# Kernel optimization log

Measured on AMD Instinct MI355X. Metric: run time of the kernel, lower is better.

The kernel has to match this reference:

```python
import jax, jax.numpy as jnp
import numpy as np

COMPRESSION = 2  # max-pool factor along flattened spatial axis for phi and g


def setup_inputs() -> dict:
    key = jax.random.key(0)
    ks = jax.random.split(key, 5)
    B, C, H, W = 4, 64, 96, 96
    Ci = 32  # intermediate_dim = C // 2
    s = 1.0 / np.sqrt(C)
    return {
        "x": jax.random.normal(ks[0], (B, C, H, W), dtype=jnp.float32),
        "w_theta": jax.random.normal(ks[1], (Ci, C), dtype=jnp.float32) * s,
        "b_theta": jnp.zeros((Ci,), dtype=jnp.float32),
        "w_phi": jax.random.normal(ks[2], (Ci, C), dtype=jnp.float32) * s,
        "b_phi": jnp.zeros((Ci,), dtype=jnp.float32),
        "w_g": jax.random.normal(ks[3], (Ci, C), dtype=jnp.float32) * s,
        "b_g": jnp.zeros((Ci,), dtype=jnp.float32),
        "w_out": jax.random.normal(ks[4], (C, Ci), dtype=jnp.float32) * (1.0 / np.sqrt(Ci)),
        "b_out": jnp.zeros((C,), dtype=jnp.float32),
    }


def reference(x, w_theta, b_theta, w_phi, b_phi, w_g, b_g, w_out, b_out):
    B, C, H, W = x.shape
    N = H * W
    xf = x.reshape(B, C, N).transpose(0, 2, 1)            # [B, N, C]
    # 1x1 conv projections == channel matmuls
    theta = xf @ w_theta.T + b_theta                      # [B, N, Ci]
    phi = xf @ w_phi.T + b_phi                            # [B, N, Ci]
    g = xf @ w_g.T + b_g                                  # [B, N, Ci]
    # compression: max-pool (kernel=stride=COMPRESSION) along flattened spatial axis
    Ci = theta.shape[-1]
    phi = phi.reshape(B, N // COMPRESSION, COMPRESSION, Ci).max(axis=2)  # [B, N/c, Ci]
    g = g.reshape(B, N // COMPRESSION, COMPRESSION, Ci).max(axis=2)      # [B, N/c, Ci]
    # embedded-gaussian affinity + softmax
    attn = jax.nn.softmax(jnp.einsum('bnc,bmc->bnm', theta, phi), axis=-1)  # [B, N, N/c]
    y = jnp.einsum('bnm,bmc->bnc', attn, g)               # [B, N, Ci]
    out = y @ w_out.T + b_out                             # [B, N, C]
    out = out.transpose(0, 2, 1).reshape(B, C, H, W)
    return out + x  # residual
```

## Files before the change

kernel.cpp:

```cpp
#include <hip/hip_runtime.h>
#include <hip/hip_bf16.h>


#define NQ 9216
#define MM 4608
#define LOG2E 1.44269504088896340736f

typedef __attribute__((ext_vector_type(8))) short bf16x8;
typedef __attribute__((ext_vector_type(4))) float f32x4;
typedef __attribute__((ext_vector_type(4))) unsigned short u16x4;

static __device__ __forceinline__ unsigned pk2(float a, float b) {
    __hip_bfloat162 h = __float22bfloat162_rn(make_float2(a, b));
    return *reinterpret_cast<unsigned*>(&h);
}

__global__ __launch_bounds__(256, 4) void proj_kernel(
    const float* __restrict__ x,
    const float* __restrict__ wt, const float* __restrict__ bt,
    const float* __restrict__ wp, const float* __restrict__ bp,
    const float* __restrict__ wg, const float* __restrict__ bg,
    unsigned short* __restrict__ theta, unsigned short* __restrict__ phi,
    unsigned short* __restrict__ gT, float* __restrict__ pzero)
{
    __shared__ unsigned short gst[32 * 20];

    const int tid  = threadIdx.x;
    const int wid  = tid >> 6;
    const int lane = tid & 63;
    const int q = lane >> 4;
    const int c = lane & 15;
    const int role = wid >> 1;
    const int sub  = wid & 1;

    {
        const int gs = gridDim.x * blockDim.x;
        float4 z4 = {0.f, 0.f, 0.f, 0.f};
        for (int i = blockIdx.x * blockDim.x + tid; i < 304128; i += gs)
            ((float4*)pzero)[i] = z4;
    }

    const int b     = blockIdx.x / 288;
    const int rem   = blockIdx.x % 288;
    const int n0blk = rem * 32;
    const int n0    = n0blk + sub * 16;

    bf16x8 af[2];
#pragma unroll
    for (int ks = 0; ks < 2; ++ks) {
        unsigned* ap = (unsigned*)&af[ks];
#pragma unroll
        for (int j2 = 0; j2 < 4; ++j2) {
            float x0 = x[(b * 64 + ks * 32 + q * 8 + j2 * 2) * NQ + n0 + c];
            float x1 = x[(b * 64 + ks * 32 + q * 8 + j2 * 2 + 1) * NQ + n0 + c];
            ap[j2] = pk2(x0, x1);
        }
    }

    if (role == 0) {
        bf16x8 wf[2][2];
        float bias[2];
#pragma unroll
        for (int ct = 0; ct < 2; ++ct) {
            bias[ct] = bt[ct * 16 + c];
#pragma unroll
            for (int ks = 0; ks < 2; ++ks) {
                const float* wsrc = wt + (ct * 16 + c) * 64 + ks * 32 + q * 8;
                f32x4 w0 = *(const f32x4*)wsrc;
                f32x4 w1 = *(const f32x4*)(wsrc + 4);
                unsigned* wk = (unsigned*)&wf[ct][ks];
                wk[0] = pk2(w0[0], w0[1]); wk[1] = pk2(w0[2], w0[3]);
                wk[2] = pk2(w1[0], w1[1]); wk[3] = pk2(w1[2], w1[3]);
            }
        }
#pragma unroll
        for (int ct = 0; ct < 2; ++ct) {
            f32x4 acc = {0.f, 0.f, 0.f, 0.f};
            acc = __builtin_amdgcn_mfma_f32_16x16x32_bf16(af[0], wf[ct][0], acc, 0, 0, 0);
            acc = __builtin_amdgcn_mfma_f32_16x16x32_bf16(af[1], wf[ct][1], acc, 0, 0, 0);
            const int ci = ct * 16 + c;
            unsigned pv0 = pk2((acc[0] + bias[ct]) * LOG2E, (acc[1] + bias[ct]) * LOG2E);
            unsigned pv1 = pk2((acc[2] + bias[ct]) * LOG2E, (acc[3] + bias[ct]) * LOG2E);
            theta[(b * NQ + n0 + 4 * q + 0) * 32 + ci] = (unsigned short)pv0;
            theta[(b * NQ + n0 + 4 * q + 1) * 32 + ci] = (unsigned short)(pv0 >> 16);
            theta[(b * NQ + n0 + 4 * q + 2) * 32 + ci] = (unsigned short)pv1;
            theta[(b * NQ + n0 + 4 * q + 3) * 32 + ci] = (unsigned short)(pv1 >> 16);
        }
    } else {
        const float* Wm[2] = {wp, wg};
        const float* Bm[2] = {bp, bg};
        bf16x8 wf[2][2][2];
        float bias[2][2];
#pragma unroll
        for (int p = 0; p < 2; ++p) {
#pragma unroll
            for (int ct = 0; ct < 2; ++ct) {
                bias[p][ct] = Bm[p][ct * 16 + c];
#pragma unroll
                for (int ks = 0; ks < 2; ++ks) {
                    const float* wsrc = Wm[p] + (ct * 16 + c) * 64 + ks * 32 + q * 8;
                    f32x4 w0 = *(const f32x4*)wsrc;
                    f32x4 w1 = *(const f32x4*)(wsrc + 4);
                    unsigned* wk = (unsigned*)&wf[p][ct][ks];
                    wk[0] = pk2(w0[0], w0[1]); wk[1] = pk2(w0[2], w0[3]);
                    wk[2] = pk2(w1[0], w1[1]); wk[3] = pk2(w1[2], w1[3]);
                }
            }
        }
#pragma unroll
        for (int p = 0; p < 2; ++p) {
#pragma unroll
            for (int ct = 0; ct < 2; ++ct) {
                f32x4 acc = {0.f, 0.f, 0.f, 0.f};
                acc = __builtin_amdgcn_mfma_f32_16x16x32_bf16(af[0], wf[p][ct][0], acc, 0, 0, 0);
                acc = __builtin_amdgcn_mfma_f32_16x16x32_bf16(af[1], wf[p][ct][1], acc, 0, 0, 0);
#pragma unroll
                for (int r = 0; r < 4; ++r) acc[r] += bias[p][ct];
                const int ci = ct * 16 + c;
                unsigned pv = pk2(fmaxf(acc[0], acc[1]), fmaxf(acc[2], acc[3]));
                if (p == 0) {
                    const int m0 = (n0 >> 1) + 2 * q;
                    phi[(b * MM + m0) * 32 + ci]     = (unsigned short)pv;
                    phi[(b * MM + m0 + 1) * 32 + ci] = (unsigned short)(pv >> 16);
                } else {
                    *(unsigned int*)(gst + ci * 20 + sub * 8 + 2 * q) = pv;
                }
            }
        }
    }

    __syncthreads();
    if (tid < 128) {
        const int ci = tid >> 2;
        const int m4 = (tid & 3) * 4;
        u16x4 v = *(const u16x4*)(gst + ci * 20 + m4);
        *(u16x4*)(gT + (b * 32 + ci) * MM + (n0blk >> 1) + m4) = v;
    }
}

__global__ __launch_bounds__(128, 4) void attn_kernel(
    const unsigned short* __restrict__ theta, const unsigned short* __restrict__ phi,
    const unsigned short* __restrict__ gT,
    float* __restrict__ pacc, float* __restrict__ plsum)
{
    __shared__ unsigned short pld[2][64 * 64];

    const int tid  = threadIdx.x;
    const int w    = tid >> 6;
    const int lane = tid & 63;
    const int q  = lane >> 4;
    const int c  = lane & 15;
    const int xr = (c & 7) << 3;

    const int ks  = blockIdx.x / 288;
    const int rem = blockIdx.x % 288;
    const int b   = rem / 72;
    const int nb  = (rem % 72) * 128 + w * 64;

    bf16x8 qf[4];
#pragma unroll
    for (int rt = 0; rt < 4; ++rt)
        qf[rt] = *(const bf16x8*)(theta + (b * NQ + nb + rt * 16 + c) * 32 + q * 8);

    bf16x8 onef;
    {
        unsigned v = (c == 0) ? 0x3F803F80u : 0u;
        unsigned* op = (unsigned*)&onef;
        op[0] = v; op[1] = v; op[2] = v; op[3] = v;
    }

    const unsigned short* phiB = phi + (size_t)b * MM * 32;
    const unsigned short* gTB  = gT + (size_t)b * 32 * MM;
    unsigned short* myp = pld[w];

    f32x4 acc[4][2];
    f32x4 lacc[4];
#pragma unroll
    for (int rt = 0; rt < 4; ++rt) {
        lacc[rt] = (f32x4){0.f, 0.f, 0.f, 0.f};
#pragma unroll
        for (int s2 = 0; s2 < 2; ++s2) acc[rt][s2] = (f32x4){0.f, 0.f, 0.f, 0.f};
    }

    const int mt0 = ks * 6;
    bf16x8 kf[4], vf[2][2];

#pragma unroll
    for (int mct = 0; mct < 4; ++mct)
        kf[mct] = *(const bf16x8*)(phiB + (mt0 * 64 + mct * 16 + c) * 32 + q * 8);
#pragma unroll
    for (int s2 = 0; s2 < 2; ++s2)
#pragma unroll
        for (int st = 0; st < 2; ++st)
            vf[s2][st] = *(const bf16x8*)(gTB + (s2 * 16 + c) * MM + mt0 * 64 + st * 32 + q * 8);
#pragma unroll
    for (int mct = 0; mct < 4; ++mct) {
#pragma unroll
        for (int rt = 0; rt < 4; ++rt) {
            f32x4 z = {0.f, 0.f, 0.f, 0.f};
            f32x4 s = __builtin_amdgcn_mfma_f32_16x16x32_bf16(kf[mct], qf[rt], z, 0, 0, 0);
            uint2 hv = {pk2(__builtin_amdgcn_exp2f(s[0]), __builtin_amdgcn_exp2f(s[1])),
                        pk2(__builtin_amdgcn_exp2f(s[2]), __builtin_amdgcn_exp2f(s[3]))};
            *(uint2*)(myp + ((rt * 16 + c) << 6) + ((mct * 16 + 4 * q) ^ xr)) = hv;
        }
    }

    for (int mi = 1; mi < 6; ++mi) {
        const int m0 = (mt0 + mi) * 64;

#pragma unroll
        for (int mct = 0; mct < 4; ++mct)
            kf[mct] = *(const bf16x8*)(phiB + (m0 + mct * 16 + c) * 32 + q * 8);

#pragma unroll
        for (int rt = 0; rt < 4; ++rt) {
#pragma unroll
            for (int st = 0; st < 2; ++st) {
                bf16x8 pf = *(const bf16x8*)(myp + ((rt * 16 + c) << 6) + ((st * 32 + q * 8) ^ xr));
#pragma unroll
                for (int s2 = 0; s2 < 2; ++s2)
                    acc[rt][s2] = __builtin_amdgcn_mfma_f32_16x16x32_bf16(vf[s2][st], pf, acc[rt][s2], 0, 0, 0);
                lacc[rt] = __builtin_amdgcn_mfma_f32_16x16x32_bf16(onef, pf, lacc[rt], 0, 0, 0);
            }
        }

#pragma unroll
        for (int s2 = 0; s2 < 2; ++s2)
#pragma unroll
            for (int st = 0; st < 2; ++st)
                vf[s2][st] = *(const bf16x8*)(gTB + (s2 * 16 + c) * MM + m0 + st * 32 + q * 8);

#pragma unroll
        for (int mct = 0; mct < 4; ++mct) {
#pragma unroll
            for (int rt = 0; rt < 4; ++rt) {
                f32x4 z = {0.f, 0.f, 0.f, 0.f};
                f32x4 s = __builtin_amdgcn_mfma_f32_16x16x32_bf16(kf[mct], qf[rt], z, 0, 0, 0);
                uint2 hv = {pk2(__builtin_amdgcn_exp2f(s[0]), __builtin_amdgcn_exp2f(s[1])),
                            pk2(__builtin_amdgcn_exp2f(s[2]), __builtin_amdgcn_exp2f(s[3]))};
                *(uint2*)(myp + ((rt * 16 + c) << 6) + ((mct * 16 + 4 * q) ^ xr)) = hv;
            }
        }
    }

#pragma unroll
    for (int rt = 0; rt < 4; ++rt) {
#pragma unroll
        for (int st = 0; st < 2; ++st) {
            bf16x8 pf = *(const bf16x8*)(myp + ((rt * 16 + c) << 6) + ((st * 32 + q * 8) ^ xr));
#pragma unroll
            for (int s2 = 0; s2 < 2; ++s2)
                acc[rt][s2] = __builtin_amdgcn_mfma_f32_16x16x32_bf16(vf[s2][st], pf, acc[rt][s2], 0, 0, 0);
            lacc[rt] = __builtin_amdgcn_mfma_f32_16x16x32_bf16(onef, pf, lacc[rt], 0, 0, 0);
        }
    }

#pragma unroll
    for (int rt = 0; rt < 4; ++rt)
#pragma unroll
        for (int s2 = 0; s2 < 2; ++s2)
#pragma unroll
            for (int r = 0; r < 4; ++r)
                atomicAdd(&pacc[(size_t)(b * 32 + s2 * 16 + 4 * q + r) * NQ + nb + rt * 16 + c],
                          acc[rt][s2][r]);
    if (lane < 16) {
#pragma unroll
        for (int rt = 0; rt < 4; ++rt)
            atomicAdd(&plsum[(size_t)b * NQ + nb + rt * 16 + lane], lacc[rt][0]);
    }
}

__global__ __launch_bounds__(128, 4) void reduce_kernel(
    const float* __restrict__ pacc, const float* __restrict__ plsum,
    const float* __restrict__ w_out, const float* __restrict__ b_out,
    const float* __restrict__ x, float* __restrict__ out)
{
    __shared__ unsigned short yld[32 * 36];

    const int tid = threadIdx.x;
    const int b   = blockIdx.x / 288;
    const int nb  = (blockIdx.x % 288) * 32;

    {
        const int ci = tid >> 2;
        const int n8 = (tid & 3) * 8;
        const float* pr = pacc + (size_t)(b * 32 + ci) * NQ + nb + n8;
        f32x4 a0 = *(const f32x4*)pr;
        f32x4 a1 = *(const f32x4*)(pr + 4);
        const float* lr = plsum + (size_t)b * NQ + nb + n8;
        f32x4 l0 = *(const f32x4*)lr;
        f32x4 l1 = *(const f32x4*)(lr + 4);
        uint2 v0 = {pk2(a0[0] / l0[0], a0[1] / l0[1]), pk2(a0[2] / l0[2], a0[3] / l0[3])};
        uint2 v1 = {pk2(a1[0] / l1[0], a1[1] / l1[1]), pk2(a1[2] / l1[2], a1[3] / l1[3])};
        *(uint2*)(yld + ci * 36 + n8)     = v0;
        *(uint2*)(yld + ci * 36 + n8 + 4) = v1;
    }
    __syncthreads();

    const int w    = tid >> 6;
    const int lane = tid & 63;
    const int q = lane >> 4;
    const int c = lane & 15;

    bf16x8 wof[4];
#pragma unroll
    for (int ct = 0; ct < 4; ++ct) {
        const float* wsrc = w_out + (ct * 16 + c) * 32 + q * 8;
        f32x4 w0 = *(const f32x4*)wsrc;
        f32x4 w1 = *(const f32x4*)(wsrc + 4);
        unsigned* wk = (unsigned*)&wof[ct];
        wk[0] = pk2(w0[0], w0[1]); wk[1] = pk2(w0[2], w0[3]);
        wk[2] = pk2(w1[0], w1[1]); wk[3] = pk2(w1[2], w1[3]);
    }

    bf16x8 yf;
    {
        unsigned short* yp = (unsigned short*)&yf;
#pragma unroll
        for (int j = 0; j < 8; ++j)
            yp[j] = yld[(q * 8 + j) * 36 + w * 16 + c];
    }

#pragma unroll
    for (int ct = 0; ct < 4; ++ct) {
        f32x4 z = {0.f, 0.f, 0.f, 0.f};
        f32x4 o = __builtin_amdgcn_mfma_f32_16x16x32_bf16(wof[ct], yf, z, 0, 0, 0);
#pragma unroll
        for (int r = 0; r < 4; ++r) {
            const int chn = ct * 16 + 4 * q + r;
            const size_t addr = (size_t)(b * 64 + chn) * NQ + nb + w * 16 + c;
            out[addr] = o[r] + b_out[chn] + x[addr];
        }
    }
}

extern "C" void kernel_launch(void* const* d_in, const int* in_sizes, int n_in,
                              void* d_out, int out_size, void* d_ws, size_t ws_size,
                              hipStream_t stream) {
    const float* x       = (const float*)d_in[0];
    const float* w_theta = (const float*)d_in[1];
    const float* b_theta = (const float*)d_in[2];
    const float* w_phi   = (const float*)d_in[3];
    const float* b_phi   = (const float*)d_in[4];
    const float* w_g     = (const float*)d_in[5];
    const float* b_g     = (const float*)d_in[6];
    const float* w_out   = (const float*)d_in[7];
    const float* b_out   = (const float*)d_in[8];
    float* out = (float*)d_out;

    unsigned short* theta = (unsigned short*)d_ws;
    unsigned short* phi   = theta + 4 * NQ * 32;
    unsigned short* gT    = phi + 4 * MM * 32;
    float* pacc  = (float*)(gT + 4 * 32 * MM);
    float* plsum = pacc + (size_t)4 * 32 * NQ;

    proj_kernel<<<1152, 256, 0, stream>>>(x, w_theta, b_theta, w_phi, b_phi,
                                          w_g, b_g, theta, phi, gT, pacc);
    attn_kernel<<<12 * 288, 128, 0, stream>>>(theta, phi, gT, pacc, plsum);
    reduce_kernel<<<1152, 128, 0, stream>>>(pacc, plsum, w_out, b_out, x, out);
}
```

Measured before the change: 151.4 us.

## Fuse output projection into attention kernel via last-block counter and resplit keys

```diff
diff --git a/kernel.cpp b/kernel.cpp
--- a/kernel.cpp
+++ b/kernel.cpp
@@ -36,7 +36,7 @@
     {
         const int gs = gridDim.x * blockDim.x;
         float4 z4 = {0.f, 0.f, 0.f, 0.f};
-        for (int i = blockIdx.x * blockDim.x + tid; i < 304128; i += gs)
+        for (int i = blockIdx.x * blockDim.x + tid; i < 304200; i += gs)
             ((float4*)pzero)[i] = z4;
     }
 
@@ -138,12 +138,15 @@
     }
 }
 
-__global__ __launch_bounds__(128, 4) void attn_kernel(
+__global__ __launch_bounds__(128, 3) void attn_kernel(
     const unsigned short* __restrict__ theta, const unsigned short* __restrict__ phi,
-    const unsigned short* __restrict__ gT,
-    float* __restrict__ pacc, float* __restrict__ plsum)
+    const unsigned short* __restrict__ gT, const float* __restrict__ w_out,
+    const float* __restrict__ b_out, const float* __restrict__ x,
+    float* __restrict__ pacc, float* __restrict__ plsum, int* __restrict__ cnt,
+    float* __restrict__ out)
 {
     __shared__ unsigned short pld[2][64 * 64];
+    __shared__ int lastSh;
 
     const int tid  = threadIdx.x;
     const int w    = tid >> 6;
@@ -155,7 +158,8 @@
     const int ks  = blockIdx.x / 288;
     const int rem = blockIdx.x % 288;
     const int b   = rem / 72;
-    const int nb  = (rem % 72) * 128 + w * 64;
+    const int qb  = rem % 72;
+    const int nb  = qb * 128 + w * 64;
 
     bf16x8 qf[4];
 #pragma unroll
@@ -182,7 +186,7 @@
         for (int s2 = 0; s2 < 2; ++s2) acc[rt][s2] = (f32x4){0.f, 0.f, 0.f, 0.f};
     }
 
-    const int mt0 = ks * 6;
+    const int mt0 = ks * 9;
     bf16x8 kf[4], vf[2][2];
 
 #pragma unroll
@@ -205,7 +209,7 @@
         }
     }
 
-    for (int mi = 1; mi < 6; ++mi) {
+    for (int mi = 1; mi < 9; ++mi) {
         const int m0 = (mt0 + mi) * 64;
 
 #pragma unroll
@@ -268,39 +272,16 @@
         for (int rt = 0; rt < 4; ++rt)
             atomicAdd(&plsum[(size_t)b * NQ + nb + rt * 16 + lane], lacc[rt][0]);
     }
-}
-
-__global__ __launch_bounds__(128, 4) void reduce_kernel(
-    const float* __restrict__ pacc, const float* __restrict__ plsum,
-    const float* __restrict__ w_out, const float* __restrict__ b_out,
-    const float* __restrict__ x, float* __restrict__ out)
-{
-    __shared__ unsigned short yld[32 * 36];
-
-    const int tid = threadIdx.x;
-    const int b   = blockIdx.x / 288;
-    const int nb  = (blockIdx.x % 288) * 32;
-
-    {
-        const int ci = tid >> 2;
-        const int n8 = (tid & 3) * 8;
-        const float* pr = pacc + (size_t)(b * 32 + ci) * NQ + nb + n8;
-        f32x4 a0 = *(const f32x4*)pr;
-        f32x4 a1 = *(const f32x4*)(pr + 4);
-        const float* lr = plsum + (size_t)b * NQ + nb + n8;
-        f32x4 l0 = *(const f32x4*)lr;
-        f32x4 l1 = *(const f32x4*)(lr + 4);
-        uint2 v0 = {pk2(a0[0] / l0[0], a0[1] / l0[1]), pk2(a0[2] / l0[2], a0[3] / l0[3])};
-        uint2 v1 = {pk2(a1[0] / l1[0], a1[1] / l1[1]), pk2(a1[2] / l1[2], a1[3] / l1[3])};
-        *(uint2*)(yld + ci * 36 + n8)     = v0;
-        *(uint2*)(yld + ci * 36 + n8 + 4) = v1;
-    }
+
     __syncthreads();
-
-    const int w    = tid >> 6;
-    const int lane = tid & 63;
-    const int q = lane >> 4;
-    const int c = lane & 15;
+    if (tid == 0) {
+        __threadfence();
+        int old = __hip_atomic_fetch_add(&cnt[rem], 1, __ATOMIC_ACQ_REL,
+                                         __HIP_MEMORY_SCOPE_AGENT);
+        lastSh = (old == 7);
+    }
+    __syncthreads();
+    if (!lastSh) return;
 
     bf16x8 wof[4];
 #pragma unroll
@@ -313,24 +294,46 @@
         wk[2] = pk2(w1[0], w1[1]); wk[3] = pk2(w1[2], w1[3]);
     }
 
-    bf16x8 yf;
-    {
-        unsigned short* yp = (unsigned short*)&yf;
-#pragma unroll
-        for (int j = 0; j < 8; ++j)
-            yp[j] = yld[(q * 8 + j) * 36 + w * 16 + c];
-    }
-
-#pragma unroll
-    for (int ct = 0; ct < 4; ++ct) {
-        f32x4 z = {0.f, 0.f, 0.f, 0.f};
-        f32x4 o = __builtin_amdgcn_mfma_f32_16x16x32_bf16(wof[ct], yf, z, 0, 0, 0);
-#pragma unroll
-        for (int r = 0; r < 4; ++r) {
-            const int chn = ct * 16 + 4 * q + r;
-            const size_t addr = (size_t)(b * 64 + chn) * NQ + nb + w * 16 + c;
-            out[addr] = o[r] + b_out[chn] + x[addr];
-        }
+    unsigned short* yld = pld[0];
+    for (int chunk = 0; chunk < 4; ++chunk) {
+        const int nb0 = qb * 128 + chunk * 32;
+        {
+            const int ci = tid >> 2;
+            const int n8 = (tid & 3) * 8;
+            const float* pr = pacc + (size_t)(b * 32 + ci) * NQ + nb0 + n8;
+            const float* lr = plsum + (size_t)b * NQ + nb0 + n8;
+            float a[8], l[8];
+#pragma unroll
+            for (int j = 0; j < 8; ++j) {
+                a[j] = __hip_atomic_load(pr + j, __ATOMIC_RELAXED, __HIP_MEMORY_SCOPE_AGENT);
+                l[j] = __hip_atomic_load(lr + j, __ATOMIC_RELAXED, __HIP_MEMORY_SCOPE_AGENT);
+            }
+            uint2 v0 = {pk2(a[0] / l[0], a[1] / l[1]), pk2(a[2] / l[2], a[3] / l[3])};
+            uint2 v1 = {pk2(a[4] / l[4], a[5] / l[5]), pk2(a[6] / l[6], a[7] / l[7])};
+            *(uint2*)(yld + ci * 36 + n8)     = v0;
+            *(uint2*)(yld + ci * 36 + n8 + 4) = v1;
+        }
+        __syncthreads();
+
+        bf16x8 yf;
+        {
+            unsigned short* yp = (unsigned short*)&yf;
+#pragma unroll
+            for (int j = 0; j < 8; ++j)
+                yp[j] = yld[(q * 8 + j) * 36 + w * 16 + c];
+        }
+#pragma unroll
+        for (int ct = 0; ct < 4; ++ct) {
+            f32x4 z = {0.f, 0.f, 0.f, 0.f};
+            f32x4 o = __builtin_amdgcn_mfma_f32_16x16x32_bf16(wof[ct], yf, z, 0, 0, 0);
+#pragma unroll
+            for (int r = 0; r < 4; ++r) {
+                const int chn = ct * 16 + 4 * q + r;
+                const size_t addr = (size_t)(b * 64 + chn) * NQ + nb0 + w * 16 + c;
+                out[addr] = o[r] + b_out[chn] + x[addr];
+            }
+        }
+        __syncthreads();
     }
 }
 
@@ -353,9 +356,10 @@
     unsigned short* gT    = phi + 4 * MM * 32;
     float* pacc  = (float*)(gT + 4 * 32 * MM);
     float* plsum = pacc + (size_t)4 * 32 * NQ;
+    int*   cnt   = (int*)(plsum + (size_t)4 * NQ);
 
     proj_kernel<<<1152, 256, 0, stream>>>(x, w_theta, b_theta, w_phi, b_phi,
                                           w_g, b_g, theta, phi, gT, pacc);
-    attn_kernel<<<12 * 288, 128, 0, stream>>>(theta, phi, gT, pacc, plsum);
-    reduce_kernel<<<1152, 128, 0, stream>>>(pacc, plsum, w_out, b_out, x, out);
+    attn_kernel<<<8 * 288, 128, 0, stream>>>(theta, phi, gT, w_out, b_out, x,
+                                             pacc, plsum, cnt, out);
 }
```

After: 232.0 us. 53.2% more time.

## Split attention tile into two row-halves to interleave softmax-exp and PV MFMAs

Applied to the files above, without the earlier changes.

```diff
diff --git a/kernel.cpp b/kernel.cpp
--- a/kernel.cpp
+++ b/kernel.cpp
@@ -13,6 +13,42 @@
 static __device__ __forceinline__ unsigned pk2(float a, float b) {
     __hip_bfloat162 h = __float22bfloat162_rn(make_float2(a, b));
     return *reinterpret_cast<unsigned*>(&h);
+}
+
+template <int R0>
+static __device__ __forceinline__ void s_half(
+    const bf16x8* kf, const bf16x8* qf, unsigned short* stg,
+    int c, int q, int xr)
+{
+#pragma unroll
+    for (int mct = 0; mct < 4; ++mct) {
+#pragma unroll
+        for (int rr = 0; rr < 2; ++rr) {
+            f32x4 z = {0.f, 0.f, 0.f, 0.f};
+            f32x4 s = __builtin_amdgcn_mfma_f32_16x16x32_bf16(kf[mct], qf[R0 + rr], z, 0, 0, 0);
+            uint2 hv = {pk2(__builtin_amdgcn_exp2f(s[0]), __builtin_amdgcn_exp2f(s[1])),
+                        pk2(__builtin_amdgcn_exp2f(s[2]), __builtin_amdgcn_exp2f(s[3]))};
+            *(uint2*)(stg + ((rr * 16 + c) << 6) + ((mct * 16 + 4 * q) ^ xr)) = hv;
+        }
+    }
+}
+
+template <int R0>
+static __device__ __forceinline__ void pv_half(
+    const bf16x8 (&vf)[2][2], const bf16x8& onef, const unsigned short* stg,
+    int c, int q, int xr, f32x4 (&acc)[4][2], f32x4 (&lacc)[4])
+{
+#pragma unroll
+    for (int rr = 0; rr < 2; ++rr) {
+#pragma unroll
+        for (int st = 0; st < 2; ++st) {
+            bf16x8 pf = *(const bf16x8*)(stg + ((rr * 16 + c) << 6) + ((st * 32 + q * 8) ^ xr));
+#pragma unroll
+            for (int s2 = 0; s2 < 2; ++s2)
+                acc[R0 + rr][s2] = __builtin_amdgcn_mfma_f32_16x16x32_bf16(vf[s2][st], pf, acc[R0 + rr][s2], 0, 0, 0);
+            lacc[R0 + rr] = __builtin_amdgcn_mfma_f32_16x16x32_bf16(onef, pf, lacc[R0 + rr], 0, 0, 0);
+        }
+    }
 }
 
 __global__ __launch_bounds__(256, 4) void proj_kernel(
@@ -138,12 +174,12 @@
     }
 }
 
-__global__ __launch_bounds__(128, 4) void attn_kernel(
+__global__ __launch_bounds__(128, 3) void attn_kernel(
     const unsigned short* __restrict__ theta, const unsigned short* __restrict__ phi,
     const unsigned short* __restrict__ gT,
     float* __restrict__ pacc, float* __restrict__ plsum)
 {
-    __shared__ unsigned short pld[2][64 * 64];
+    __shared__ unsigned short pld[2][2][32 * 64];
 
     const int tid  = threadIdx.x;
     const int w    = tid >> 6;
@@ -171,7 +207,8 @@
 
     const unsigned short* phiB = phi + (size_t)b * MM * 32;
     const unsigned short* gTB  = gT + (size_t)b * 32 * MM;
-    unsigned short* myp = pld[w];
+    unsigned short* stg0 = pld[w][0];
+    unsigned short* stg1 = pld[w][1];
 
     f32x4 acc[4][2];
     f32x4 lacc[4];
@@ -182,78 +219,43 @@
         for (int s2 = 0; s2 < 2; ++s2) acc[rt][s2] = (f32x4){0.f, 0.f, 0.f, 0.f};
     }
 
-    const int mt0 = ks * 6;
+    const int mt0 = ks * 9;
     bf16x8 kf[4], vf[2][2];
 
 #pragma unroll
     for (int mct = 0; mct < 4; ++mct)
         kf[mct] = *(const bf16x8*)(phiB + (mt0 * 64 + mct * 16 + c) * 32 + q * 8);
+    s_half<0>(kf, qf, stg0, c, q, xr);
 #pragma unroll
     for (int s2 = 0; s2 < 2; ++s2)
 #pragma unroll
         for (int st = 0; st < 2; ++st)
             vf[s2][st] = *(const bf16x8*)(gTB + (s2 * 16 + c) * MM + mt0 * 64 + st * 32 + q * 8);
-#pragma unroll
-    for (int mct = 0; mct < 4; ++mct) {
-#pragma unroll
-        for (int rt = 0; rt < 4; ++rt) {
-            f32x4 z = {0.f, 0.f, 0.f, 0.f};
-            f32x4 s = __builtin_amdgcn_mfma_f32_16x16x32_bf16(kf[mct], qf[rt], z, 0, 0, 0);
-            uint2 hv = {pk2(__builtin_amdgcn_exp2f(s[0]), __builtin_amdgcn_exp2f(s[1])),
-                        pk2(__builtin_amdgcn_exp2f(s[2]), __builtin_amdgcn_exp2f(s[3]))};
-            *(uint2*)(myp + ((rt * 16 + c) << 6) + ((mct * 16 + 4 * q) ^ xr)) = hv;
-        }
-    }
-
-    for (int mi = 1; mi < 6; ++mi) {
-        const int m0 = (mt0 + mi) * 64;
-
-#pragma unroll
-        for (int mct = 0; mct < 4; ++mct)
-            kf[mct] = *(const bf16x8*)(phiB + (m0 + mct * 16 + c) * 32 + q * 8);
-
-#pragma unroll
-        for (int rt = 0; rt < 4; ++rt) {
-#pragma unroll
-            for (int st = 0; st < 2; ++st) {
-                bf16x8 pf = *(const bf16x8*)(myp + ((rt * 16 + c) << 6) + ((st * 32 + q * 8) ^ xr));
-#pragma unroll
-                for (int s2 = 0; s2 < 2; ++s2)
-                    acc[rt][s2] = __builtin_amdgcn_mfma_f32_16x16x32_bf16(vf[s2][st], pf, acc[rt][s2], 0, 0, 0);
-                lacc[rt] = __builtin_amdgcn_mfma_f32_16x16x32_bf16(onef, pf, lacc[rt], 0, 0, 0);
-            }
-        }
-
+    s_half<2>(kf, qf, stg1, c, q, xr);
+#pragma unroll
+    for (int mct = 0; mct < 4; ++mct)
+        kf[mct] = *(const bf16x8*)(phiB + ((mt0 + 1) * 64 + mct * 16 + c) * 32 + q * 8);
+    pv_half<0>(vf, onef, stg0, c, q, xr, acc, lacc);
+
+    for (int mi = 1; mi < 9; ++mi) {
+        const int m0  = (mt0 + mi) * 64;
+        const int m0n = (mt0 + (mi < 8 ? mi + 1 : mi)) * 64;
+
+        s_half<0>(kf, qf, stg0, c, q, xr);
+        pv_half<2>(vf, onef, stg1, c, q, xr, acc, lacc);
 #pragma unroll
         for (int s2 = 0; s2 < 2; ++s2)
 #pragma unroll
             for (int st = 0; st < 2; ++st)
                 vf[s2][st] = *(const bf16x8*)(gTB + (s2 * 16 + c) * MM + m0 + st * 32 + q * 8);
-
-#pragma unroll
-        for (int mct = 0; mct < 4; ++mct) {
-#pragma unroll
-            for (int rt = 0; rt < 4; ++rt) {
-                f32x4 z = {0.f, 0.f, 0.f, 0.f};
-                f32x4 s = __builtin_amdgcn_mfma_f32_16x16x32_bf16(kf[mct], qf[rt], z, 0, 0, 0);
-                uint2 hv = {pk2(__builtin_amdgcn_exp2f(s[0]), __builtin_amdgcn_exp2f(s[1])),
-                            pk2(__builtin_amdgcn_exp2f(s[2]), __builtin_amdgcn_exp2f(s[3]))};
-                *(uint2*)(myp + ((rt * 16 + c) << 6) + ((mct * 16 + 4 * q) ^ xr)) = hv;
-            }
-        }
-    }
-
-#pragma unroll
-    for (int rt = 0; rt < 4; ++rt) {
-#pragma unroll
-        for (int st = 0; st < 2; ++st) {
-            bf16x8 pf = *(const bf16x8*)(myp + ((rt * 16 + c) << 6) + ((st * 32 + q * 8) ^ xr));
-#pragma unroll
-            for (int s2 = 0; s2 < 2; ++s2)
-                acc[rt][s2] = __builtin_amdgcn_mfma_f32_16x16x32_bf16(vf[s2][st], pf, acc[rt][s2], 0, 0, 0);
-            lacc[rt] = __builtin_amdgcn_mfma_f32_16x16x32_bf16(onef, pf, lacc[rt], 0, 0, 0);
-        }
-    }
+        s_half<2>(kf, qf, stg1, c, q, xr);
+#pragma unroll
+        for (int mct = 0; mct < 4; ++mct)
+            kf[mct] = *(const bf16x8*)(phiB + (m0n + mct * 16 + c) * 32 + q * 8);
+        pv_half<0>(vf, onef, stg0, c, q, xr, acc, lacc);
+    }
+
+    pv_half<2>(vf, onef, stg1, c, q, xr, acc, lacc);
 
 #pragma unroll
     for (int rt = 0; rt < 4; ++rt)
@@ -356,6 +358,6 @@
 
     proj_kernel<<<1152, 256, 0, stream>>>(x, w_theta, b_theta, w_phi, b_phi,
                                           w_g, b_g, theta, phi, gT, pacc);
-    attn_kernel<<<12 * 288, 128, 0, stream>>>(theta, phi, gT, pacc, plsum);
+    attn_kernel<<<8 * 288, 128, 0, stream>>>(theta, phi, gT, pacc, plsum);
     reduce_kernel<<<1152, 128, 0, stream>>>(pacc, plsum, w_out, b_out, x, out);
 }
```

Result: no change. 149.3 us (-1.4%).

## Halve query tile per wave, lengthen key split, rotate key-tile start order

Applied to the files above, without the earlier changes.

```diff
diff --git a/kernel.cpp b/kernel.cpp
--- a/kernel.cpp
+++ b/kernel.cpp
@@ -138,12 +138,12 @@
     }
 }
 
-__global__ __launch_bounds__(128, 4) void attn_kernel(
+__global__ __launch_bounds__(128, 6) void attn_kernel(
     const unsigned short* __restrict__ theta, const unsigned short* __restrict__ phi,
     const unsigned short* __restrict__ gT,
     float* __restrict__ pacc, float* __restrict__ plsum)
 {
-    __shared__ unsigned short pld[2][64 * 64];
+    __shared__ unsigned short pld[2][32 * 64];
 
     const int tid  = threadIdx.x;
     const int w    = tid >> 6;
@@ -152,14 +152,15 @@
     const int c  = lane & 15;
     const int xr = (c & 7) << 3;
 
-    const int ks  = blockIdx.x / 288;
-    const int rem = blockIdx.x % 288;
-    const int b   = rem / 72;
-    const int nb  = (rem % 72) * 128 + w * 64;
-
-    bf16x8 qf[4];
-#pragma unroll
-    for (int rt = 0; rt < 4; ++rt)
+    const int ks  = blockIdx.x / 576;
+    const int rem = blockIdx.x % 576;
+    const int b   = rem / 144;
+    const int qb  = rem % 144;
+    const int nb  = qb * 64 + w * 32;
+
+    bf16x8 qf[2];
+#pragma unroll
+    for (int rt = 0; rt < 2; ++rt)
         qf[rt] = *(const bf16x8*)(theta + (b * NQ + nb + rt * 16 + c) * 32 + q * 8);
 
     bf16x8 onef;
@@ -173,81 +174,102 @@
     const unsigned short* gTB  = gT + (size_t)b * 32 * MM;
     unsigned short* myp = pld[w];
 
-    f32x4 acc[4][2];
-    f32x4 lacc[4];
-#pragma unroll
-    for (int rt = 0; rt < 4; ++rt) {
+    unsigned short* wadr[4];
+#pragma unroll
+    for (int mct = 0; mct < 4; ++mct)
+        wadr[mct] = myp + (c << 6) + ((mct * 16 + 4 * q) ^ xr);
+    const unsigned short* radr[2];
+#pragma unroll
+    for (int st = 0; st < 2; ++st)
+        radr[st] = myp + (c << 6) + ((st * 32 + q * 8) ^ xr);
+
+    const int ofsK = c * 32 + q * 8;
+    const int ofsV = c * MM + q * 8;
+
+    f32x4 acc[2][2];
+    f32x4 lacc[2];
+#pragma unroll
+    for (int rt = 0; rt < 2; ++rt) {
         lacc[rt] = (f32x4){0.f, 0.f, 0.f, 0.f};
 #pragma unroll
         for (int s2 = 0; s2 < 2; ++s2) acc[rt][s2] = (f32x4){0.f, 0.f, 0.f, 0.f};
     }
 
-    const int mt0 = ks * 6;
+    const int mt0 = ks * 9;
+    const int rot = blockIdx.x % 9;
     bf16x8 kf[4], vf[2][2];
 
-#pragma unroll
-    for (int mct = 0; mct < 4; ++mct)
-        kf[mct] = *(const bf16x8*)(phiB + (mt0 * 64 + mct * 16 + c) * 32 + q * 8);
-#pragma unroll
-    for (int s2 = 0; s2 < 2; ++s2)
-#pragma unroll
-        for (int st = 0; st < 2; ++st)
-            vf[s2][st] = *(const bf16x8*)(gTB + (s2 * 16 + c) * MM + mt0 * 64 + st * 32 + q * 8);
-#pragma unroll
-    for (int mct = 0; mct < 4; ++mct) {
-#pragma unroll
-        for (int rt = 0; rt < 4; ++rt) {
-            f32x4 z = {0.f, 0.f, 0.f, 0.f};
-            f32x4 s = __builtin_amdgcn_mfma_f32_16x16x32_bf16(kf[mct], qf[rt], z, 0, 0, 0);
-            uint2 hv = {pk2(__builtin_amdgcn_exp2f(s[0]), __builtin_amdgcn_exp2f(s[1])),
-                        pk2(__builtin_amdgcn_exp2f(s[2]), __builtin_amdgcn_exp2f(s[3]))};
-            *(uint2*)(myp + ((rt * 16 + c) << 6) + ((mct * 16 + 4 * q) ^ xr)) = hv;
-        }
-    }
-
-    for (int mi = 1; mi < 6; ++mi) {
-        const int m0 = (mt0 + mi) * 64;
-
+    {
+        const int mt = mt0 + rot;
+        const unsigned short* pk = phiB + mt * 2048;
+        const unsigned short* pv = gTB + mt * 64;
 #pragma unroll
         for (int mct = 0; mct < 4; ++mct)
-            kf[mct] = *(const bf16x8*)(phiB + (m0 + mct * 16 + c) * 32 + q * 8);
-
-#pragma unroll
-        for (int rt = 0; rt < 4; ++rt) {
-#pragma unroll
-            for (int st = 0; st < 2; ++st) {
-                bf16x8 pf = *(const bf16x8*)(myp + ((rt * 16 + c) << 6) + ((st * 32 + q * 8) ^ xr));
-#pragma unroll
-                for (int s2 = 0; s2 < 2; ++s2)
-                    acc[rt][s2] = __builtin_amdgcn_mfma_f32_16x16x32_bf16(vf[s2][st], pf, acc[rt][s2], 0, 0, 0);
-                lacc[rt] = __builtin_amdgcn_mfma_f32_16x16x32_bf16(onef, pf, lacc[rt], 0, 0, 0);
-            }
-        }
-
+            kf[mct] = *(const bf16x8*)(pk + mct * 512 + ofsK);
 #pragma unroll
         for (int s2 = 0; s2 < 2; ++s2)
 #pragma unroll
             for (int st = 0; st < 2; ++st)
-                vf[s2][st] = *(const bf16x8*)(gTB + (s2 * 16 + c) * MM + m0 + st * 32 + q * 8);
-
+                vf[s2][st] = *(const bf16x8*)(pv + s2 * 16 * MM + st * 32 + ofsV);
 #pragma unroll
         for (int mct = 0; mct < 4; ++mct) {
 #pragma unroll
-            for (int rt = 0; rt < 4; ++rt) {
+            for (int rt = 0; rt < 2; ++rt) {
                 f32x4 z = {0.f, 0.f, 0.f, 0.f};
                 f32x4 s = __builtin_amdgcn_mfma_f32_16x16x32_bf16(kf[mct], qf[rt], z, 0, 0, 0);
                 uint2 hv = {pk2(__builtin_amdgcn_exp2f(s[0]), __builtin_amdgcn_exp2f(s[1])),
                             pk2(__builtin_amdgcn_exp2f(s[2]), __builtin_amdgcn_exp2f(s[3]))};
-                *(uint2*)(myp + ((rt * 16 + c) << 6) + ((mct * 16 + 4 * q) ^ xr)) = hv;
-            }
-        }
-    }
-
-#pragma unroll
-    for (int rt = 0; rt < 4; ++rt) {
+                *(uint2*)(wadr[mct] + rt * 1024) = hv;
+            }
+        }
+    }
+
+    for (int idx = 1; idx < 9; ++idx) {
+        int mi = idx + rot; if (mi >= 9) mi -= 9;
+        const int mt = mt0 + mi;
+        const unsigned short* pk = phiB + mt * 2048;
+        const unsigned short* pv = gTB + mt * 64;
+
+#pragma unroll
+        for (int mct = 0; mct < 4; ++mct)
+            kf[mct] = *(const bf16x8*)(pk + mct * 512 + ofsK);
+
+#pragma unroll
+        for (int rt = 0; rt < 2; ++rt) {
+#pragma unroll
+            for (int st = 0; st < 2; ++st) {
+                bf16x8 pf = *(const bf16x8*)(radr[st] + rt * 1024);
+#pragma unroll
+                for (int s2 = 0; s2 < 2; ++s2)
+                    acc[rt][s2] = __builtin_amdgcn_mfma_f32_16x16x32_bf16(vf[s2][st], pf, acc[rt][s2], 0, 0, 0);
+                lacc[rt] = __builtin_amdgcn_mfma_f32_16x16x32_bf16(onef, pf, lacc[rt], 0, 0, 0);
+            }
+        }
+
+#pragma unroll
+        for (int s2 = 0; s2 < 2; ++s2)
+#pragma unroll
+            for (int st = 0; st < 2; ++st)
+                vf[s2][st] = *(const bf16x8*)(pv + s2 * 16 * MM + st * 32 + ofsV);
+
+#pragma unroll
+        for (int mct = 0; mct < 4; ++mct) {
+#pragma unroll
+            for (int rt = 0; rt < 2; ++rt) {
+                f32x4 z = {0.f, 0.f, 0.f, 0.f};
+                f32x4 s = __builtin_amdgcn_mfma_f32_16x16x32_bf16(kf[mct], qf[rt], z, 0, 0, 0);
+                uint2 hv = {pk2(__builtin_amdgcn_exp2f(s[0]), __builtin_amdgcn_exp2f(s[1])),
+                            pk2(__builtin_amdgcn_exp2f(s[2]), __builtin_amdgcn_exp2f(s[3]))};
+                *(uint2*)(wadr[mct] + rt * 1024) = hv;
+            }
+        }
+    }
+
+#pragma unroll
+    for (int rt = 0; rt < 2; ++rt) {
 #pragma unroll
         for (int st = 0; st < 2; ++st) {
-            bf16x8 pf = *(const bf16x8*)(myp + ((rt * 16 + c) << 6) + ((st * 32 + q * 8) ^ xr));
+            bf16x8 pf = *(const bf16x8*)(radr[st] + rt * 1024);
 #pragma unroll
             for (int s2 = 0; s2 < 2; ++s2)
                 acc[rt][s2] = __builtin_amdgcn_mfma_f32_16x16x32_bf16(vf[s2][st], pf, acc[rt][s2], 0, 0, 0);
@@ -256,7 +278,7 @@
     }
 
 #pragma unroll
-    for (int rt = 0; rt < 4; ++rt)
+    for (int rt = 0; rt < 2; ++rt)
 #pragma unroll
         for (int s2 = 0; s2 < 2; ++s2)
 #pragma unroll
@@ -265,7 +287,7 @@
                           acc[rt][s2][r]);
     if (lane < 16) {
 #pragma unroll
-        for (int rt = 0; rt < 4; ++rt)
+        for (int rt = 0; rt < 2; ++rt)
             atomicAdd(&plsum[(size_t)b * NQ + nb + rt * 16 + lane], lacc[rt][0]);
     }
 }
@@ -356,6 +378,6 @@
 
     proj_kernel<<<1152, 256, 0, stream>>>(x, w_theta, b_theta, w_phi, b_phi,
                                           w_g, b_g, theta, phi, gT, pacc);
-    attn_kernel<<<12 * 288, 128, 0, stream>>>(theta, phi, gT, pacc, plsum);
+    attn_kernel<<<8 * 576, 128, 0, stream>>>(theta, phi, gT, pacc, plsum);
     reduce_kernel<<<1152, 128, 0, stream>>>(pacc, plsum, w_out, b_out, x, out);
 }
```

After: 175.1 us. +15.6%, slower.
